# Performance work log

Hardware: AMD Instinct MI355X
Metric: run time of the kernel (lower is better)

Reference implementation:

```python
import jax, jax.numpy as jnp
import numpy as np

WS = 7          # window size (fixed: last_idx=169=(2*7-1)^2)
NP = 1          # num_priorset
NH = 8          # num heads
DIM = 256
SHIFT = 3
N = WS * WS     # 49 tokens per window
NK = N + 3 * NP # 52 K/V tokens (window + uk/fg/bg priors)


def _rel_index():
    coords = np.stack(np.meshgrid(np.arange(WS), np.arange(WS), indexing='ij')).reshape(2, -1)
    rel = (coords[:, :, None] - coords[:, None, :]).transpose(1, 2, 0).astype(np.int64)
    rel[:, :, 0] += WS - 1
    rel[:, :, 1] += WS - 1
    rel[:, :, 0] *= 2 * WS - 1
    idx = rel.sum(-1)                      # (49,49) in [0,168]
    full = np.full((N, NK), 169, dtype=np.int64)
    full[:, :N] = idx
    for j in range(3 * NP):
        full[:, N + j] = 169 + j           # dedicated bias rows for priors
    return jnp.asarray(full)

REL_IDX = _rel_index()


def _ln(t, g, b, eps=1e-5):
    mu = t.mean(-1, keepdims=True)
    var = ((t - mu) ** 2).mean(-1, keepdims=True)
    return (t - mu) * jax.lax.rsqrt(var + eps) * g + b


def setup_inputs() -> dict:
    key = jax.random.key(0)
    ks = jax.random.split(key, 16)
    B, H, W, C = 4, 112, 112, DIM
    nW = (H // WS) * (W // WS)
    hid = 4 * C
    inp = {
        'x': jax.random.normal(ks[0], (B, H * W, C), jnp.float32),
        'mask_matrix': jax.random.normal(ks[1], (nW, N, N), jnp.float32),
        'area_fg': jax.random.uniform(ks[2], (B, H, W, 1), jnp.float32),
        'area_bg': jax.random.uniform(ks[3], (B, H, W, 1), jnp.float32),
        'area_uk': jax.random.uniform(ks[4], (B, H, W, 1), jnp.float32),
        'norm1_g': jnp.ones((C,), jnp.float32),
        'norm1_b': jnp.zeros((C,), jnp.float32),
        'norm2_g': jnp.ones((C,), jnp.float32),
        'norm2_b': jnp.zeros((C,), jnp.float32),
        'qkv_w': jax.random.normal(ks[5], (3 * C, C), jnp.float32) * 0.02,
        'qkv_b': jnp.zeros((3 * C,), jnp.float32),
        'proj_w': jax.random.normal(ks[6], (C, C), jnp.float32) * 0.02,
        'proj_b': jnp.zeros((C,), jnp.float32),
        'rel_table': jax.random.normal(ks[7], (169 + 3 * NP, NH), jnp.float32) * 0.02,
        'fc1_w': jax.random.normal(ks[8], (hid, C), jnp.float32) * 0.02,
        'fc1_b': jnp.zeros((hid,), jnp.float32),
        'fc2_w': jax.random.normal(ks[9], (C, hid), jnp.float32) * 0.02,
        'fc2_b': jnp.zeros((C,), jnp.float32),
        'H': 112,
        'W': 112,
    }
    return inp


def reference(x, mask_matrix, area_fg, area_bg, area_uk,
              norm1_g, norm1_b, norm2_g, norm2_b,
              qkv_w, qkv_b, proj_w, proj_b, rel_table,
              fc1_w, fc1_b, fc2_w, fc2_b, H, W):
    B, L, C = x.shape
    d = C // NH
    scale = d ** -0.5
    nWh, nWw = H // WS, W // WS
    nW = nWh * nWw

    shortcut = x
    x4 = x.reshape(B, H, W, C)
    eps = 1e-9
    # masked global-average prior tokens (B, C)
    def pooled(area):
        return (area * x4).sum((1, 2)) / (area.sum((1, 2)) + eps)
    uk, fg, bg = pooled(area_uk), pooled(area_fg), pooled(area_bg)

    xn = _ln(x, norm1_g, norm1_b).reshape(B, H, W, C)
    uk_n = _ln(uk, norm1_g, norm1_b)
    fg_n = _ln(fg, norm1_g, norm1_b)
    bg_n = _ln(bg, norm1_g, norm1_b)

    # cyclic shift + window partition (H,W divisible by WS -> no padding)
    xs = jnp.roll(xn, (-SHIFT, -SHIFT), (1, 2))
    xw = xs.reshape(B, nWh, WS, nWw, WS, C).transpose(0, 1, 3, 2, 4, 5).reshape(B * nW, N, C)

    # prior highway tokens (order: unknown, fg, bg) and per-window copies
    ph = jnp.stack([uk_n, fg_n, bg_n], axis=1)                      # (B,3,C)
    pr = jnp.broadcast_to(ph[:, None], (B, nW, 3, C)).reshape(B * nW, 3, C)
    xk = jnp.concatenate([xw, pr], axis=1)                          # (B_,52,C)

    qkv = (xk @ qkv_w.T + qkv_b).reshape(B * nW, NK, 3, NH, d)
    q = qkv[:, :N, 0].transpose(0, 2, 1, 3) * scale                 # (B_,h,49,d)
    k = qkv[:, :, 1].transpose(0, 2, 1, 3)                          # (B_,h,52,d)
    v = qkv[:, :, 2].transpose(0, 2, 1, 3)

    attn = jnp.einsum('bhnd,bhmd->bhnm', q, k)                      # (B_,h,49,52)
    bias = rel_table[REL_IDX].transpose(2, 0, 1)                    # (h,49,52)
    attn = attn + bias[None]
    mask = jnp.pad(mask_matrix, ((0, 0), (0, 0), (0, 3 * NP)))      # (nW,49,52)
    attn = attn.reshape(B, nW, NH, N, NK) + mask[None, :, None]
    attn = jax.nn.softmax(attn.reshape(B * nW, NH, N, NK), axis=-1)

    out = jnp.einsum('bhnm,bhmd->bhnd', attn, v)
    out = out.transpose(0, 2, 1, 3).reshape(B * nW, N, C)
    out = out @ proj_w.T + proj_b

    # prior highway: qkv on priors, keep V, project
    ph_qkv = (ph @ qkv_w.T + qkv_b).reshape(B, 3 * NP, 3, NH, d)
    v_hw = ph_qkv[:, :, 2].reshape(B, 3 * NP, C) @ proj_w.T + proj_b

    # window reverse + reverse shift
    xo = out.reshape(B, nWh, nWw, WS, WS, C).transpose(0, 1, 3, 2, 4, 5).reshape(B, H, W, C)
    xo = jnp.roll(xo, (SHIFT, SHIFT), (1, 2)).reshape(B, L, C)

    x = shortcut + xo
    h = _ln(x, norm2_g, norm2_b)
    h = jax.nn.gelu(h @ fc1_w.T + fc1_b, approximate=False)
    x = x + (h @ fc2_w.T + fc2_b)
    return x, v_hw
```

## Files before the change

### kernel.cpp

```cpp
#include <hip/hip_runtime.h>
#include <hip/hip_bf16.h>
#include <math.h>

typedef __bf16 bf16;
typedef bf16 bf16x8 __attribute__((ext_vector_type(8)));
typedef bf16 bf16x4 __attribute__((ext_vector_type(4)));
typedef float f32x4 __attribute__((ext_vector_type(4)));

constexpr int DIM   = 256;
constexpr int NH    = 8;
constexpr int LTOT  = 112 * 112;
constexpr int BTOT  = 4;
constexpr int MROWS = BTOT * LTOT;
constexpr int MQKV  = MROWS + BTOT * 3;
constexpr int NTOK  = 49;
constexpr int NKV   = 52;

__global__ void cvt_f32_bf16(const float* __restrict__ s, bf16* __restrict__ d, int n) {
    int i = blockIdx.x * 256 + threadIdx.x;
    if (i < n) d[i] = (bf16)s[i];
}

__global__ __launch_bounds__(256) void pool_partial(
    const float* __restrict__ x, const float* __restrict__ afg,
    const float* __restrict__ abg, const float* __restrict__ auk,
    float* __restrict__ pnum, float* __restrict__ pden)
{
    int b = blockIdx.x / 49, ch = blockIdx.x % 49;
    int p0 = ch * 256, tid = threadIdx.x;
    __shared__ float su[256], sf[256], sb[256];
    int p = p0 + tid;
    su[tid] = auk[b * LTOT + p];
    sf[tid] = afg[b * LTOT + p];
    sb[tid] = abg[b * LTOT + p];
    __syncthreads();
    float nu = 0.f, nf = 0.f, nb = 0.f;
    const float* xp = x + ((size_t)b * LTOT + p0) * DIM + tid;
    for (int pp = 0; pp < 256; ++pp) {
        float xv = xp[(size_t)pp * DIM];
        nu += su[pp] * xv; nf += sf[pp] * xv; nb += sb[pp] * xv;
    }
    size_t base = (size_t)blockIdx.x * 3 * DIM + tid;
    pnum[base]           = nu;
    pnum[base + DIM]     = nf;
    pnum[base + 2 * DIM] = nb;
    if (tid < 3) {
        const float* sptr = tid == 0 ? su : (tid == 1 ? sf : sb);
        float t = 0.f;
        for (int i = 0; i < 256; ++i) t += sptr[i];
        pden[blockIdx.x * 3 + tid] = t;
    }
}

__device__ __forceinline__ void block_meanvar(float v, float& mu, float& rstd, float eps) {
    float s = v, s2 = v * v;
    #pragma unroll
    for (int o = 32; o >= 1; o >>= 1) { s += __shfl_down(s, o); s2 += __shfl_down(s2, o); }
    __shared__ float ps[4], ps2[4];
    int w = threadIdx.x >> 6, ln = threadIdx.x & 63;
    if (ln == 0) { ps[w] = s; ps2[w] = s2; }
    __syncthreads();
    float S  = ps[0] + ps[1] + ps[2] + ps[3];
    float S2 = ps2[0] + ps2[1] + ps2[2] + ps2[3];
    mu = S * (1.f / 256.f);
    float var = S2 * (1.f / 256.f) - mu * mu;
    rstd = rsqrtf(var + eps);
}

__global__ __launch_bounds__(256) void prior_ln(
    const float* __restrict__ pnum, const float* __restrict__ pden,
    const float* __restrict__ g, const float* __restrict__ bt, bf16* __restrict__ xn)
{
    int b = blockIdx.x / 3, j = blockIdx.x % 3, tid = threadIdx.x;
    float s = 0.f, den = 0.f;
    for (int ch = 0; ch < 49; ++ch) {
        s   += pnum[((size_t)(b * 49 + ch) * 3 + j) * DIM + tid];
        den += pden[(b * 49 + ch) * 3 + j];
    }
    float v = s / (den + 1e-9f);
    float mu, rs;
    block_meanvar(v, mu, rs, 1e-5f);
    xn[((size_t)MROWS + blockIdx.x) * DIM + tid] = (bf16)((v - mu) * rs * g[tid] + bt[tid]);
}

__global__ __launch_bounds__(256) void ln1_kernel(
    const float* __restrict__ x, const float* __restrict__ g,
    const float* __restrict__ bt, bf16* __restrict__ xn)
{
    size_t row = blockIdx.x; int tid = threadIdx.x;
    float v = x[row * DIM + tid];
    float mu, rs;
    block_meanvar(v, mu, rs, 1e-5f);
    xn[row * DIM + tid] = (bf16)((v - mu) * rs * g[tid] + bt[tid]);
}

__device__ __forceinline__ void load_lds16(const void* g, void* l) {
    __builtin_amdgcn_global_load_lds((const __attribute__((address_space(1))) void*)g,
                                     (__attribute__((address_space(3))) void*)l, 16, 0, 0);
}

template <int EPI>
__global__ __launch_bounds__(256) void gemm_bt(
    const bf16* __restrict__ A, const bf16* __restrict__ W,
    const float* __restrict__ bias, bf16* __restrict__ Cb,
    float* __restrict__ Cf, const float* __restrict__ resid,
    int M, int N, int K)
{
    __shared__ __align__(16) char smem[49152];
    const int tid = threadIdx.x;
    const int wv = tid >> 6, lane = tid & 63;

    const int gx = gridDim.x;
    const int nwg = gx * (int)gridDim.y;
    int lin = blockIdx.y * gx + blockIdx.x;
    int xcd = lin & 7, loc = lin >> 3;
    int qq = nwg >> 3, rr = nwg & 7;
    int nid = (xcd < rr ? xcd * (qq + 1) : rr * (qq + 1) + (xcd - rr) * qq) + loc;
    int by = nid / gx, bx = nid - by * gx;
    const int m0 = by * 128, n0 = bx * 128;

    const int r  = tid >> 2;
    const int kb = (((tid & 3) ^ ((tid >> 3) & 3)) * 8);
    const int wr = (wv >> 1) * 64, wc = (wv & 1) * 64;
    const int fr = lane & 15;
    const int fo = (((lane >> 4) ^ ((fr >> 1) & 3)) * 8);

    int ra0 = m0 + r;      if (ra0 >= M) ra0 = M - 1;
    int ra1 = m0 + r + 64; if (ra1 >= M) ra1 = M - 1;
    const bf16* pA0 = A + (size_t)ra0 * K + kb;
    const bf16* pA1 = A + (size_t)ra1 * K + kb;
    const bf16* pW0 = W + (size_t)(n0 + r) * K + kb;
    const bf16* pW1 = W + (size_t)(n0 + r + 64) * K + kb;

    const f32x4 zero = {0.f, 0.f, 0.f, 0.f};
    f32x4 acc[4][4];
    #pragma unroll
    for (int i = 0; i < 4; ++i)
        #pragma unroll
        for (int j = 0; j < 4; ++j) acc[i][j] = zero;

    const int nK = K >> 5;

    auto stage = [&](int kt, int b) {
        bf16* Ab = (bf16*)(smem + b * 16384);
        bf16* Bb = (bf16*)(smem + b * 16384 + 8192);
        const int off = kt * 32;
        load_lds16(pA0 + off, Ab + wv * 512);
        load_lds16(pA1 + off, Ab + 2048 + wv * 512);
        load_lds16(pW0 + off, Bb + wv * 512);
        load_lds16(pW1 + off, Bb + 2048 + wv * 512);
    };

    stage(0, 0);
    stage(1, 1);

    int cur = 0;
    for (int kt = 0; kt < nK; ++kt) {
        asm volatile("s_waitcnt lgkmcnt(0)" ::: "memory");
        if (kt < nK - 1) asm volatile("s_waitcnt vmcnt(4)" ::: "memory");
        else             asm volatile("s_waitcnt vmcnt(0)" ::: "memory");
        __builtin_amdgcn_s_barrier();
        if (kt + 2 < nK) {
            int nb = cur + 2; if (nb >= 3) nb -= 3;
            stage(kt + 2, nb);
        }
        const bf16* Ac = (const bf16*)(smem + cur * 16384);
        const bf16* Bc = (const bf16*)(smem + cur * 16384 + 8192);
        bf16x8 af[4], bw[4];
        #pragma unroll
        for (int i = 0; i < 4; ++i) af[i] = *(const bf16x8*)(Ac + (wr + i * 16 + fr) * 32 + fo);
        #pragma unroll
        for (int i = 0; i < 4; ++i) bw[i] = *(const bf16x8*)(Bc + (wc + i * 16 + fr) * 32 + fo);
        #pragma unroll
        for (int i = 0; i < 4; ++i)
            #pragma unroll
            for (int j = 0; j < 4; ++j)
                acc[i][j] = __builtin_amdgcn_mfma_f32_16x16x32_bf16(af[i], bw[j], acc[i][j], 0, 0, 0);
        ++cur; if (cur == 3) cur = 0;
    }
    __syncthreads();

    const int cr = (lane >> 4) * 4, cc = lane & 15;
    if constexpr (EPI == 3) {
        float* Cs = (float*)smem;
        #pragma unroll
        for (int half = 0; half < 2; ++half) {
            if (wr == half * 64) {
                #pragma unroll
                for (int i = 0; i < 4; ++i)
                    #pragma unroll
                    for (int j = 0; j < 4; ++j) {
                        const int col = wc + j * 16 + cc;
                        const float bv = bias[n0 + col];
                        #pragma unroll
                        for (int q = 0; q < 4; ++q)
                            Cs[(i * 16 + cr + q) * 132 + col] = acc[i][j][q] + bv;
                    }
            }
            __syncthreads();
            for (int p = tid; p < 2048; p += 256) {
                const int row = p >> 5, seg = (p & 31) * 4;
                const int gr = m0 + half * 64 + row;
                if (gr < M) {
                    f32x4 v = *(const f32x4*)(Cs + row * 132 + seg);
                    const size_t o = (size_t)gr * N + n0 + seg;
                    f32x4 rv = *(const f32x4*)(resid + o);
                    *(f32x4*)(Cf + o) = v + rv;
                }
            }
            __syncthreads();
        }
    } else {
        bf16* Csb = (bf16*)smem;
        #pragma unroll
        for (int i = 0; i < 4; ++i)
            #pragma unroll
            for (int j = 0; j < 4; ++j) {
                const int col = wc + j * 16 + cc;
                const float bv = bias[n0 + col];
                #pragma unroll
                for (int q = 0; q < 4; ++q) {
                    float v = acc[i][j][q] + bv;
                    if constexpr (EPI == 2) {
                        float u = 0.7978845608028654f * (v + 0.044715f * v * v * v);
                        v = v / (1.f + __expf(-2.f * u));
                    }
                    Csb[(wr + i * 16 + cr + q) * 144 + col] = (bf16)v;
                }
            }
        __syncthreads();
        for (int p = tid; p < 2048; p += 256) {
            const int row = p >> 4, seg = (p & 15) * 8;
            const int gr = m0 + row;
            if (gr < M)
                *(bf16x8*)(Cb + (size_t)gr * N + n0 + seg) = *(const bf16x8*)(Csb + row * 144 + seg);
        }
    }
}

__global__ __launch_bounds__(256) void proj_ln2(
    const bf16* __restrict__ A, const bf16* __restrict__ W,
    const float* __restrict__ bias, const float* __restrict__ x,
    const float* __restrict__ g, const float* __restrict__ bt,
    float* __restrict__ x2, bf16* __restrict__ ln2)
{
    __shared__ __align__(16) char smem[40960];
    bf16* As = (bf16*)smem;
    bf16* Bs = (bf16*)(smem + 8192);

    const int tid = threadIdx.x;
    const int wv = tid >> 6, lane = tid & 63;
    const int m0 = blockIdx.x * 64;

    const int r4 = tid >> 2;
    const int kb = (((tid & 3) ^ ((tid >> 3) & 3)) * 8);
    const int fr = lane & 15;
    const int fo = (((lane >> 4) ^ ((fr >> 1) & 3)) * 8);

    const bf16* pA  = A + (size_t)(m0 + r4) * 256 + kb;
    const bf16* pW0 = W + (size_t)(r4)       * 256 + kb;
    const bf16* pW1 = W + (size_t)(r4 + 64)  * 256 + kb;
    const bf16* pW2 = W + (size_t)(r4 + 128) * 256 + kb;
    const bf16* pW3 = W + (size_t)(r4 + 192) * 256 + kb;

    const f32x4 zero = {0.f, 0.f, 0.f, 0.f};
    f32x4 acc[4][4];
    #pragma unroll
    for (int i = 0; i < 4; ++i)
        #pragma unroll
        for (int j = 0; j < 4; ++j) acc[i][j] = zero;

    auto stage = [&](int kt, int b) {
        const int off = kt * 32;
        load_lds16(pA  + off, As + b * 2048 + wv * 512);
        load_lds16(pW0 + off, Bs + b * 8192 + wv * 512);
        load_lds16(pW1 + off, Bs + b * 8192 + 2048 + wv * 512);
        load_lds16(pW2 + off, Bs + b * 8192 + 4096 + wv * 512);
        load_lds16(pW3 + off, Bs + b * 8192 + 6144 + wv * 512);
    };

    stage(0, 0);
    __syncthreads();
    int cur = 0;
    for (int kt = 0; kt < 8; ++kt) {
        if (kt + 1 < 8) stage(kt + 1, cur ^ 1);
        const bf16* Ac = As + cur * 2048;
        const bf16* Bc = Bs + cur * 8192;
        bf16x8 af[4], bw[4];
        #pragma unroll
        for (int i = 0; i < 4; ++i) af[i] = *(const bf16x8*)(Ac + (i * 16 + fr) * 32 + fo);
        #pragma unroll
        for (int j = 0; j < 4; ++j) bw[j] = *(const bf16x8*)(Bc + (wv * 64 + j * 16 + fr) * 32 + fo);
        #pragma unroll
        for (int i = 0; i < 4; ++i)
            #pragma unroll
            for (int j = 0; j < 4; ++j)
                acc[i][j] = __builtin_amdgcn_mfma_f32_16x16x32_bf16(af[i], bw[j], acc[i][j], 0, 0, 0);
        __syncthreads();
        cur ^= 1;
    }

    float* red = (float*)smem;
    const int cr = (lane >> 4) * 4, cc = lane & 15;

    int nrw[4][4];
    #pragma unroll
    for (int i = 0; i < 4; ++i)
        #pragma unroll
        for (int q = 0; q < 4; ++q) {
            int ar = m0 + i * 16 + cr + q;
            int bwin = ar / 49;
            int n = ar - bwin * 49;
            int bb = bwin >> 8, w = bwin & 255;
            int ni = n / 7, nj = n - ni * 7;
            int hh = (w >> 4) * 7 + ni + 3;  if (hh >= 112) hh -= 112;
            int ww2 = (w & 15) * 7 + nj + 3; if (ww2 >= 112) ww2 -= 112;
            nrw[i][q] = bb * LTOT + hh * 112 + ww2;
        }

    float s1[4][4], s2[4][4];
    #pragma unroll
    for (int i = 0; i < 4; ++i)
        #pragma unroll
        for (int q = 0; q < 4; ++q) { s1[i][q] = 0.f; s2[i][q] = 0.f; }

    #pragma unroll
    for (int j = 0; j < 4; ++j) {
        const int col = wv * 64 + j * 16 + cc;
        const float bv = bias[col];
        #pragma unroll
        for (int i = 0; i < 4; ++i)
            #pragma unroll
            for (int q = 0; q < 4; ++q) {
                float v = acc[i][j][q] + bv + x[(size_t)nrw[i][q] * 256 + col];
                acc[i][j][q] = v;
                s1[i][q] += v; s2[i][q] += v * v;
            }
    }
    #pragma unroll
    for (int o = 1; o < 16; o <<= 1)
        #pragma unroll
        for (int i = 0; i < 4; ++i)
            #pragma unroll
            for (int q = 0; q < 4; ++q) {
                s1[i][q] += __shfl_xor(s1[i][q], o);
                s2[i][q] += __shfl_xor(s2[i][q], o);
            }
    if (cc == 0) {
        #pragma unroll
        for (int i = 0; i < 4; ++i)
            #pragma unroll
            for (int q = 0; q < 4; ++q) {
                int m = i * 16 + cr + q;
                red[m * 8 + wv * 2]     = s1[i][q];
                red[m * 8 + wv * 2 + 1] = s2[i][q];
            }
    }
    __syncthreads();

    float mu[4][4], rs[4][4];
    #pragma unroll
    for (int i = 0; i < 4; ++i)
        #pragma unroll
        for (int q = 0; q < 4; ++q) {
            int m = i * 16 + cr + q;
            float S  = red[m * 8] + red[m * 8 + 2] + red[m * 8 + 4] + red[m * 8 + 6];
            float S2 = red[m * 8 + 1] + red[m * 8 + 3] + red[m * 8 + 5] + red[m * 8 + 7];
            float mm = S * (1.f / 256.f);
            float var = S2 * (1.f / 256.f) - mm * mm;
            mu[i][q] = mm;
            rs[i][q] = rsqrtf(var + 1e-5f);
        }
    #pragma unroll
    for (int j = 0; j < 4; ++j) {
        const int col = wv * 64 + j * 16 + cc;
        const float gv = g[col], bv2 = bt[col];
        #pragma unroll
        for (int i = 0; i < 4; ++i)
            #pragma unroll
            for (int q = 0; q < 4; ++q) {
                float v = acc[i][j][q];
                size_t o = (size_t)nrw[i][q] * 256 + col;
                x2[o] = v;
                ln2[o] = (bf16)((v - mu[i][q]) * rs[i][q] * gv + bv2);
            }
    }
}

__global__ __launch_bounds__(512, 1) void attn_kernel(
    const bf16* __restrict__ qkv, const float* __restrict__ mask,
    const float* __restrict__ rel, bf16* __restrict__ att_out)
{
    __shared__ int rowtab[52];
    __shared__ float mLds[64 * 67];
    __shared__ float rLds[1376];
    __shared__ __align__(16) bf16 vT[8 * 32 * 80];
    __shared__ __align__(16) bf16 pbuf[8 * 64 * 80];

    const int tid = threadIdx.x;
    const int bw = blockIdx.x;
    const int b = bw >> 8, w = bw & 255;
    const int wh = w >> 4, wwi = w & 15;

    if (tid < 52) {
        int row;
        if (tid < 49) {
            int i = tid / 7, j = tid % 7;
            int gh = wh * 7 + i + 3;  if (gh >= 112) gh -= 112;
            int gw = wwi * 7 + j + 3; if (gw >= 112) gw -= 112;
            row = b * LTOT + gh * 112 + gw;
        } else {
            row = MROWS + b * 3 + (tid - 49);
        }
        rowtab[tid] = row;
    }
    __syncthreads();

    for (int e = tid; e < 64 * 67; e += 512) {
        int q = e / 67, k = e % 67;
        mLds[e] = (q < 49 && k < 49) ? mask[(size_t)w * 2401 + q * 49 + k] : 0.f;
    }
    for (int e = tid; e < 1376; e += 512) rLds[e] = rel[e];
    for (int e = tid; e < 256 * 12; e += 512) {
        int rr = e / 12, c = 52 + e % 12;
        vT[rr * 80 + c] = (bf16)0.f;
    }
    for (int e = tid; e < 52 * 256; e += 512) {
        int key = e >> 8, c = e & 255;
        vT[c * 80 + key] = qkv[(size_t)rowtab[key] * 768 + 512 + c];
    }
    __syncthreads();

    const int h    = tid >> 6;
    const int lane = tid & 63;
    const int cl   = lane & 15;
    const int hi4  = lane >> 4;
    const int cr   = hi4 * 4;
    const int fo   = hi4 * 8;

    bf16x8 kf[4], qf[4];
    #pragma unroll
    for (int i = 0; i < 4; ++i) {
        int key = 16 * i + cl; if (key > 51) key = 51;
        kf[i] = *(const bf16x8*)(qkv + (size_t)rowtab[key] * 768 + 256 + h * 32 + fo);
    }
    #pragma unroll
    for (int j = 0; j < 4; ++j) {
        int qq = 16 * j + cl; if (qq > 48) qq = 48;
        qf[j] = *(const bf16x8*)(qkv + (size_t)rowtab[qq] * 768 + h * 32 + fo);
    }
    const f32x4 zero = {0.f, 0.f, 0.f, 0.f};
    f32x4 acc[4][4];
    #pragma unroll
    for (int i = 0; i < 4; ++i)
        #pragma unroll
        for (int j = 0; j < 4; ++j) acc[i][j] = zero;
    #pragma unroll
    for (int i = 0; i < 4; ++i)
        #pragma unroll
        for (int j = 0; j < 4; ++j)
            acc[i][j] = __builtin_amdgcn_mfma_f32_16x16x32_bf16(kf[i], qf[j], acc[i][j], 0, 0, 0);

    int kb[4][4];
    #pragma unroll
    for (int i = 0; i < 4; ++i)
        #pragma unroll
        for (int r = 0; r < 4; ++r) {
            int key = 16 * i + cr + r;
            kb[i][r] = (key / 7) * 13 + (key % 7);
        }
    bf16* pW = pbuf + h * (64 * 80);
    #pragma unroll
    for (int j = 0; j < 4; ++j) {
        const int q = 16 * j + cl;
        const int i1 = q / 7, j1 = q % 7;
        const int qb = (i1 + 6) * 13 + (j1 + 6);
        float sv[16];
        float mx = -3e38f;
        #pragma unroll
        for (int i = 0; i < 4; ++i)
            #pragma unroll
            for (int r = 0; r < 4; ++r) {
                int key = 16 * i + cr + r;
                int idx = key < 49 ? (qb - kb[i][r]) : (169 + key - 49);
                idx = idx < 0 ? 0 : (idx > 171 ? 171 : idx);
                float s = acc[i][j][r] * 0.17677669529663687f
                        + mLds[q * 67 + key] + rLds[idx * 8 + h];
                if (key >= 52) s = -3e38f;
                sv[i * 4 + r] = s;
                mx = fmaxf(mx, s);
            }
        mx = fmaxf(mx, __shfl_xor(mx, 16));
        mx = fmaxf(mx, __shfl_xor(mx, 32));
        float sum = 0.f;
        #pragma unroll
        for (int e = 0; e < 16; ++e) { float p = __expf(sv[e] - mx); sv[e] = p; sum += p; }
        sum += __shfl_xor(sum, 16);
        sum += __shfl_xor(sum, 32);
        const float inv = 1.f / sum;
        #pragma unroll
        for (int i = 0; i < 4; ++i) {
            bf16x4 pk;
            #pragma unroll
            for (int r = 0; r < 4; ++r) pk[r] = (bf16)(sv[i * 4 + r] * inv);
            *(bf16x4*)(pW + q * 80 + 16 * i + cr) = pk;
        }
    }

    f32x4 oacc[4][2];
    #pragma unroll
    for (int i = 0; i < 4; ++i) { oacc[i][0] = zero; oacc[i][1] = zero; }
    #pragma unroll
    for (int ks = 0; ks < 2; ++ks) {
        bf16x8 vf[2];
        #pragma unroll
        for (int j2 = 0; j2 < 2; ++j2)
            vf[j2] = *(const bf16x8*)(vT + (h * 32 + 16 * j2 + cl) * 80 + 32 * ks + fo);
        #pragma unroll
        for (int i = 0; i < 4; ++i) {
            bf16x8 pf = *(const bf16x8*)(pW + (16 * i + cl) * 80 + 32 * ks + fo);
            #pragma unroll
            for (int j2 = 0; j2 < 2; ++j2)
                oacc[i][j2] = __builtin_amdgcn_mfma_f32_16x16x32_bf16(pf, vf[j2], oacc[i][j2], 0, 0, 0);
        }
    }

    #pragma unroll
    for (int i = 0; i < 4; ++i)
        #pragma unroll
        for (int r = 0; r < 4; ++r) {
            int q = 16 * i + cr + r;
            if (q < 49) {
                bf16* op = att_out + ((size_t)bw * 49 + q) * 256 + h * 32 + cl;
                op[0]  = (bf16)oacc[i][0][r];
                op[16] = (bf16)oacc[i][1][r];
            }
        }
}

__global__ __launch_bounds__(256) void vhw_kernel(
    const bf16* __restrict__ qkv, const float* __restrict__ pw,
    const float* __restrict__ pb, float* __restrict__ outp)
{
    int rowI = blockIdx.x;
    int c = threadIdx.x;
    const bf16* vp = qkv + (size_t)(MROWS + rowI) * 768 + 512;
    const float* wr_ = pw + (size_t)c * DIM;
    float acc = pb[c];
    for (int k = 0; k < DIM; ++k) acc += (float)vp[k] * wr_[k];
    outp[(size_t)rowI * DIM + c] = acc;
}

extern "C" void kernel_launch(void* const* d_in, const int* in_sizes, int n_in,
                              void* d_out, int out_size, void* d_ws, size_t ws_size,
                              hipStream_t stream)
{
    const float* x     = (const float*)d_in[0];
    const float* mask  = (const float*)d_in[1];
    const float* afg   = (const float*)d_in[2];
    const float* abg   = (const float*)d_in[3];
    const float* auk   = (const float*)d_in[4];
    const float* n1g   = (const float*)d_in[5];
    const float* n1b   = (const float*)d_in[6];
    const float* n2g   = (const float*)d_in[7];
    const float* n2b   = (const float*)d_in[8];
    const float* qkvw  = (const float*)d_in[9];
    const float* qkvb  = (const float*)d_in[10];
    const float* projw = (const float*)d_in[11];
    const float* projb = (const float*)d_in[12];
    const float* rel   = (const float*)d_in[13];
    const float* fc1w  = (const float*)d_in[14];
    const float* fc1b  = (const float*)d_in[15];
    const float* fc2w  = (const float*)d_in[16];
    const float* fc2b  = (const float*)d_in[17];
    float* out = (float*)d_out;
    char*  ws  = (char*)d_ws;

    bf16*  wq   = (bf16*)(ws + 0);
    bf16*  wp   = (bf16*)(ws + 393216);
    bf16*  wf1  = (bf16*)(ws + 524288);
    bf16*  wf2  = (bf16*)(ws + 1048576);
    float* pnum = (float*)(ws + 1572864);
    float* pden = (float*)(ws + 1572864 + 602112);
    bf16* xn    = (bf16*)(ws + (2ull << 20));
    bf16* atto  = (bf16*)(ws + (2ull << 20));
    bf16* hbuf  = (bf16*)(ws + (2ull << 20));
    bf16* qkvo  = (bf16*)(ws + (28ull << 20));
    bf16* ln2b  = (bf16*)(ws + (102ull << 20));

    cvt_f32_bf16<<<(196608 + 255) / 256, 256, 0, stream>>>(qkvw, wq, 196608);
    cvt_f32_bf16<<<(65536  + 255) / 256, 256, 0, stream>>>(projw, wp, 65536);
    cvt_f32_bf16<<<(262144 + 255) / 256, 256, 0, stream>>>(fc1w, wf1, 262144);
    cvt_f32_bf16<<<(262144 + 255) / 256, 256, 0, stream>>>(fc2w, wf2, 262144);

    pool_partial<<<BTOT * 49, 256, 0, stream>>>(x, afg, abg, auk, pnum, pden);
    prior_ln<<<12, 256, 0, stream>>>(pnum, pden, n1g, n1b, xn);
    ln1_kernel<<<MROWS, 256, 0, stream>>>(x, n1g, n1b, xn);

    gemm_bt<0><<<dim3(6, 393), 256, 0, stream>>>(xn, wq, qkvb, qkvo, nullptr, nullptr, MQKV, 768, 256);

    attn_kernel<<<BTOT * 256, 512, 0, stream>>>(qkvo, mask, rel, atto);
    vhw_kernel<<<12, 256, 0, stream>>>(qkvo, projw, projb, out + (size_t)MROWS * DIM);

    proj_ln2<<<MROWS / 64, 256, 0, stream>>>(atto, wp, projb, x, n2g, n2b, out, ln2b);

    gemm_bt<2><<<dim3(8, 392), 256, 0, stream>>>(ln2b, wf1, fc1b, hbuf, nullptr, nullptr, MROWS, 1024, 256);
    gemm_bt<3><<<dim3(2, 392), 256, 0, stream>>>(hbuf, wf2, fc2b, nullptr, out, out, MROWS, 256, 1024);

    (void)in_sizes; (void)n_in; (void)out_size; (void)ws_size;
}
```

Baseline: 328.4 us.

## Fuse weight casts, widen pooling grid, vectorize LN1, templatize GEMM shapes

Merges the four weight-conversion launches into one kernel. Splits the pooling reduction into 196 chunks per batch instead of 49, which gives more parallelism; pnum/pden move into the qkv workspace region. LN1 now handles one row per wavefront, using float4 loads and xor shuffles in place of a block-wide reduction. GEMM K and N become template constants so the k-loop can be fully unrolled with static buffer indices, and the proj kernel loop is unrolled too. The trade-offs are larger code size and more partial sums for prior_ln to reduce.

```diff
diff --git a/kernel.cpp b/kernel.cpp
--- a/kernel.cpp
+++ b/kernel.cpp
@@ -16,9 +16,18 @@
 constexpr int NTOK  = 49;
 constexpr int NKV   = 52;
 
-__global__ void cvt_f32_bf16(const float* __restrict__ s, bf16* __restrict__ d, int n) {
+__global__ __launch_bounds__(256) void cvt_all(
+    const float* __restrict__ qkvw, const float* __restrict__ projw,
+    const float* __restrict__ fc1w, const float* __restrict__ fc2w,
+    bf16* __restrict__ d)
+{
     int i = blockIdx.x * 256 + threadIdx.x;
-    if (i < n) d[i] = (bf16)s[i];
+    float v;
+    if (i < 196608)      v = qkvw[i];
+    else if (i < 262144) v = projw[i - 196608];
+    else if (i < 524288) v = fc1w[i - 262144];
+    else                 v = fc2w[i - 524288];
+    d[i] = (bf16)v;
 }
 
 __global__ __launch_bounds__(256) void pool_partial(
@@ -26,17 +35,19 @@
     const float* __restrict__ abg, const float* __restrict__ auk,
     float* __restrict__ pnum, float* __restrict__ pden)
 {
-    int b = blockIdx.x / 49, ch = blockIdx.x % 49;
-    int p0 = ch * 256, tid = threadIdx.x;
-    __shared__ float su[256], sf[256], sb[256];
-    int p = p0 + tid;
-    su[tid] = auk[b * LTOT + p];
-    sf[tid] = afg[b * LTOT + p];
-    sb[tid] = abg[b * LTOT + p];
+    int b = blockIdx.x / 196, ch = blockIdx.x % 196;
+    int p0 = ch * 64, tid = threadIdx.x;
+    __shared__ float su[64], sf[64], sb[64];
+    if (tid < 64) {
+        int p = p0 + tid;
+        su[tid] = auk[b * LTOT + p];
+        sf[tid] = afg[b * LTOT + p];
+        sb[tid] = abg[b * LTOT + p];
+    }
     __syncthreads();
     float nu = 0.f, nf = 0.f, nb = 0.f;
     const float* xp = x + ((size_t)b * LTOT + p0) * DIM + tid;
-    for (int pp = 0; pp < 256; ++pp) {
+    for (int pp = 0; pp < 64; ++pp) {
         float xv = xp[(size_t)pp * DIM];
         nu += su[pp] * xv; nf += sf[pp] * xv; nb += sb[pp] * xv;
     }
@@ -47,7 +58,7 @@
     if (tid < 3) {
         const float* sptr = tid == 0 ? su : (tid == 1 ? sf : sb);
         float t = 0.f;
-        for (int i = 0; i < 256; ++i) t += sptr[i];
+        for (int i = 0; i < 64; ++i) t += sptr[i];
         pden[blockIdx.x * 3 + tid] = t;
     }
 }
@@ -73,9 +84,9 @@
 {
     int b = blockIdx.x / 3, j = blockIdx.x % 3, tid = threadIdx.x;
     float s = 0.f, den = 0.f;
-    for (int ch = 0; ch < 49; ++ch) {
-        s   += pnum[((size_t)(b * 49 + ch) * 3 + j) * DIM + tid];
-        den += pden[(b * 49 + ch) * 3 + j];
+    for (int ch = 0; ch < 196; ++ch) {
+        s   += pnum[((size_t)(b * 196 + ch) * 3 + j) * DIM + tid];
+        den += pden[(b * 196 + ch) * 3 + j];
     }
     float v = s / (den + 1e-9f);
     float mu, rs;
@@ -83,15 +94,26 @@
     xn[((size_t)MROWS + blockIdx.x) * DIM + tid] = (bf16)((v - mu) * rs * g[tid] + bt[tid]);
 }
 
-__global__ __launch_bounds__(256) void ln1_kernel(
+__global__ __launch_bounds__(512) void ln1_kernel(
     const float* __restrict__ x, const float* __restrict__ g,
     const float* __restrict__ bt, bf16* __restrict__ xn)
 {
-    size_t row = blockIdx.x; int tid = threadIdx.x;
-    float v = x[row * DIM + tid];
-    float mu, rs;
-    block_meanvar(v, mu, rs, 1e-5f);
-    xn[row * DIM + tid] = (bf16)((v - mu) * rs * g[tid] + bt[tid]);
+    const size_t row = (size_t)blockIdx.x * 8 + (threadIdx.x >> 6);
+    const int lane = threadIdx.x & 63;
+    f32x4 v = *(const f32x4*)(x + row * DIM + lane * 4);
+    float s  = v[0] + v[1] + v[2] + v[3];
+    float s2 = v[0]*v[0] + v[1]*v[1] + v[2]*v[2] + v[3]*v[3];
+    #pragma unroll
+    for (int o = 32; o >= 1; o >>= 1) { s += __shfl_xor(s, o); s2 += __shfl_xor(s2, o); }
+    float mu = s * (1.f / 256.f);
+    float var = s2 * (1.f / 256.f) - mu * mu;
+    float rs = rsqrtf(var + 1e-5f);
+    f32x4 gv = *(const f32x4*)(g + lane * 4);
+    f32x4 bv = *(const f32x4*)(bt + lane * 4);
+    bf16x4 o;
+    #pragma unroll
+    for (int u = 0; u < 4; ++u) o[u] = (bf16)((v[u] - mu) * rs * gv[u] + bv[u]);
+    *(bf16x4*)(xn + row * DIM + lane * 4) = o;
 }
 
 __device__ __forceinline__ void load_lds16(const void* g, void* l) {
@@ -99,12 +121,11 @@
                                      (__attribute__((address_space(3))) void*)l, 16, 0, 0);
 }
 
-template <int EPI>
+template <int EPI, int K, int N>
 __global__ __launch_bounds__(256) void gemm_bt(
     const bf16* __restrict__ A, const bf16* __restrict__ W,
     const float* __restrict__ bias, bf16* __restrict__ Cb,
-    float* __restrict__ Cf, const float* __restrict__ resid,
-    int M, int N, int K)
+    float* __restrict__ Cf, const float* __restrict__ resid, int M)
 {
     __shared__ __align__(16) char smem[49152];
     const int tid = threadIdx.x;
@@ -139,7 +160,7 @@
         #pragma unroll
         for (int j = 0; j < 4; ++j) acc[i][j] = zero;
 
-    const int nK = K >> 5;
+    constexpr int nK = K >> 5;
 
     auto stage = [&](int kt, int b) {
         bf16* Ab = (bf16*)(smem + b * 16384);
@@ -154,16 +175,14 @@
     stage(0, 0);
     stage(1, 1);
 
-    int cur = 0;
+    #pragma unroll
     for (int kt = 0; kt < nK; ++kt) {
+        const int cur = kt % 3;
         asm volatile("s_waitcnt lgkmcnt(0)" ::: "memory");
         if (kt < nK - 1) asm volatile("s_waitcnt vmcnt(4)" ::: "memory");
         else             asm volatile("s_waitcnt vmcnt(0)" ::: "memory");
         __builtin_amdgcn_s_barrier();
-        if (kt + 2 < nK) {
-            int nb = cur + 2; if (nb >= 3) nb -= 3;
-            stage(kt + 2, nb);
-        }
+        if (kt + 2 < nK) stage(kt + 2, (kt + 2) % 3);
         const bf16* Ac = (const bf16*)(smem + cur * 16384);
         const bf16* Bc = (const bf16*)(smem + cur * 16384 + 8192);
         bf16x8 af[4], bw[4];
@@ -176,7 +195,6 @@
             #pragma unroll
             for (int j = 0; j < 4; ++j)
                 acc[i][j] = __builtin_amdgcn_mfma_f32_16x16x32_bf16(af[i], bw[j], acc[i][j], 0, 0, 0);
-        ++cur; if (cur == 3) cur = 0;
     }
     __syncthreads();
 
@@ -281,8 +299,9 @@
 
     stage(0, 0);
     __syncthreads();
-    int cur = 0;
+    #pragma unroll
     for (int kt = 0; kt < 8; ++kt) {
+        const int cur = kt & 1;
         if (kt + 1 < 8) stage(kt + 1, cur ^ 1);
         const bf16* Ac = As + cur * 2048;
         const bf16* Bc = Bs + cur * 8192;
@@ -297,7 +316,6 @@
             for (int j = 0; j < 4; ++j)
                 acc[i][j] = __builtin_amdgcn_mfma_f32_16x16x32_bf16(af[i], bw[j], acc[i][j], 0, 0, 0);
         __syncthreads();
-        cur ^= 1;
     }
 
     float* red = (float*)smem;
@@ -580,32 +598,30 @@
     bf16*  wp   = (bf16*)(ws + 393216);
     bf16*  wf1  = (bf16*)(ws + 524288);
     bf16*  wf2  = (bf16*)(ws + 1048576);
-    float* pnum = (float*)(ws + 1572864);
-    float* pden = (float*)(ws + 1572864 + 602112);
+    float* pnum = (float*)(ws + (28ull << 20));
+    float* pden = (float*)(ws + (28ull << 20) + 2408448);
     bf16* xn    = (bf16*)(ws + (2ull << 20));
     bf16* atto  = (bf16*)(ws + (2ull << 20));
     bf16* hbuf  = (bf16*)(ws + (2ull << 20));
     bf16* qkvo  = (bf16*)(ws + (28ull << 20));
     bf16* ln2b  = (bf16*)(ws + (102ull << 20));
 
-    cvt_f32_bf16<<<(196608 + 255) / 256, 256, 0, stream>>>(qkvw, wq, 196608);
-    cvt_f32_bf16<<<(65536  + 255) / 256, 256, 0, stream>>>(projw, wp, 65536);
-    cvt_f32_bf16<<<(262144 + 255) / 256, 256, 0, stream>>>(fc1w, wf1, 262144);
-    cvt_f32_bf16<<<(262144 + 255) / 256, 256, 0, stream>>>(fc2w, wf2, 262144);
-
-    pool_partial<<<BTOT * 49, 256, 0, stream>>>(x, afg, abg, auk, pnum, pden);
+    cvt_all<<<3072, 256, 0, stream>>>(qkvw, projw, fc1w, fc2w, (bf16*)ws);
+
+    pool_partial<<<BTOT * 196, 256, 0, stream>>>(x, afg, abg, auk, pnum, pden);
     prior_ln<<<12, 256, 0, stream>>>(pnum, pden, n1g, n1b, xn);
-    ln1_kernel<<<MROWS, 256, 0, stream>>>(x, n1g, n1b, xn);
-
-    gemm_bt<0><<<dim3(6, 393), 256, 0, stream>>>(xn, wq, qkvb, qkvo, nullptr, nullptr, MQKV, 768, 256);
+    ln1_kernel<<<MROWS / 8, 512, 0, stream>>>(x, n1g, n1b, xn);
+
+    gemm_bt<0, 256, 768><<<dim3(6, 393), 256, 0, stream>>>(xn, wq, qkvb, qkvo, nullptr, nullptr, MQKV);
 
     attn_kernel<<<BTOT * 256, 512, 0, stream>>>(qkvo, mask, rel, atto);
     vhw_kernel<<<12, 256, 0, stream>>>(qkvo, projw, projb, out + (size_t)MROWS * DIM);
 
     proj_ln2<<<MROWS / 64, 256, 0, stream>>>(atto, wp, projb, x, n2g, n2b, out, ln2b);
 
-    gemm_bt<2><<<dim3(8, 392), 256, 0, stream>>>(ln2b, wf1, fc1b, hbuf, nullptr, nullptr, MROWS, 1024, 256);
-    gemm_bt<3><<<dim3(2, 392), 256, 0, stream>>>(hbuf, wf2, fc2b, nullptr, out, out, MROWS, 256, 1024);
+    gemm_bt<2, 256, 1024><<<dim3(8, 392), 256, 0, stream>>>(ln2b, wf1, fc1b, hbuf, nullptr, nullptr, MROWS);
+
+    gemm_bt<3, 1024, 256><<<dim3(2, 392), 256, 0, stream>>>(hbuf, wf2, fc2b, nullptr, out, out, MROWS);
 
     (void)in_sizes; (void)n_in; (void)out_size; (void)ws_size;
 }
```

Measured after the change: 305.5 us. 7.0% less time.
